# Kernel optimization log

Measured on AMD Instinct MI355X. Metric: run time of the kernel, lower is better.

Reference implementation:

```python
import jax, jax.numpy as jnp
import numpy as np

B, P, ENC = 64, 196, 512
E, H, A, V, L = 1024, 1024, 512, 20000, 25


def setup_inputs() -> dict:
    key = jax.random.key(0)
    ks = jax.random.split(key, 20)
    s = 0.02
    return {
        "encoder_out": jax.random.normal(ks[0], (B, P, ENC), jnp.float32),
        "captions": jax.random.randint(ks[1], (B, L), 0, V),
        "lengths": L,
        # attention MLP
        "W_enc_att": jax.random.normal(ks[2], (ENC, A), jnp.float32) * s,
        "b_enc_att": jnp.zeros((A,), jnp.float32),
        "W_dec_att": jax.random.normal(ks[3], (H, A), jnp.float32) * s,
        "b_dec_att": jnp.zeros((A,), jnp.float32),
        "W_full_att": jax.random.normal(ks[4], (A, 1), jnp.float32) * s,
        "b_full_att": jnp.zeros((1,), jnp.float32),
        # embedding
        "emb_table": jax.random.normal(ks[5], (V, E), jnp.float32) * s,
        # LSTMCell: input = embedding + context -> (E+ENC, 4H)
        "W_ih": jax.random.normal(ks[6], (E + ENC, 4 * H), jnp.float32) * s,
        "b_ih": jnp.zeros((4 * H,), jnp.float32),
        "W_hh": jax.random.normal(ks[7], (H, 4 * H), jnp.float32) * s,
        "b_hh": jnp.zeros((4 * H,), jnp.float32),
        # init states
        "W_init_h": jax.random.normal(ks[8], (ENC, H), jnp.float32) * s,
        "b_init_h": jnp.zeros((H,), jnp.float32),
        "W_init_c": jax.random.normal(ks[9], (ENC, H), jnp.float32) * s,
        "b_init_c": jnp.zeros((H,), jnp.float32),
        # gate + output proj
        "W_fbeta": jax.random.normal(ks[10], (H, ENC), jnp.float32) * s,
        "b_fbeta": jnp.zeros((ENC,), jnp.float32),
        "W_fc": jax.random.normal(ks[11], (H, V), jnp.float32) * s,
        "b_fc": jnp.zeros((V,), jnp.float32),
    }


def _decode(encoder_out, W_enc_att, b_enc_att, W_dec_att, b_dec_att,
            W_full_att, b_full_att, emb_table, W_ih, b_ih, W_hh, b_hh,
            W_init_h, b_init_h, W_init_c, b_init_c, W_fbeta, b_fbeta,
            W_fc, b_fc, captions, T):
    # precompute encoder-side attention projection (constant across timesteps)
    att_enc = encoder_out @ W_enc_att + b_enc_att          # (B, P, A)
    mean_feat = encoder_out.mean(axis=1)                   # (B, ENC)
    h0 = mean_feat @ W_init_h + b_init_h
    c0 = mean_feat @ W_init_c + b_init_c
    embeddings = emb_table[captions[:, :T]]                # (B, T, E)
    xs = jnp.swapaxes(embeddings, 0, 1)                    # (T, B, E)

    def step(carry, emb_t):
        h, c = carry
        att_dec = h @ W_dec_att + b_dec_att                # (B, A)
        energy = (jax.nn.relu(att_enc + att_dec[:, None, :]) @ W_full_att
                  + b_full_att)[..., 0]                    # (B, P)
        alpha = jax.nn.softmax(energy, axis=1)
        context = jnp.einsum('bp,bpe->be', alpha, encoder_out)
        gate = jax.nn.sigmoid(h @ W_fbeta + b_fbeta)       # (B, ENC)
        x = jnp.concatenate([emb_t, gate * context], axis=1)
        gates = x @ W_ih + b_ih + h @ W_hh + b_hh          # (B, 4H)
        i, f, g, o = jnp.split(gates, 4, axis=1)           # torch order i,f,g,o
        c = jax.nn.sigmoid(f) * c + jax.nn.sigmoid(i) * jnp.tanh(g)
        h = jax.nn.sigmoid(o) * jnp.tanh(c)
        preds = h @ W_fc + b_fc                            # dropout = identity (eval)
        return (h, c), (preds, alpha)

    _, (preds, alphas) = jax.lax.scan(step, (h0, c0), xs)
    predictions = jnp.swapaxes(preds, 0, 1)                # (B, T, V)
    alphas = jnp.swapaxes(alphas, 0, 1)                    # (B, T, P)
    return predictions, alphas


def reference(encoder_out, captions, lengths, W_enc_att, b_enc_att, W_dec_att,
              b_dec_att, W_full_att, b_full_att, emb_table, W_ih, b_ih, W_hh,
              b_hh, W_init_h, b_init_h, W_init_c, b_init_c, W_fbeta, b_fbeta,
              W_fc, b_fc):
    T = int(lengths) - 1
    return _decode(encoder_out, W_enc_att, b_enc_att, W_dec_att, b_dec_att,
                   W_full_att, b_full_att, emb_table, W_ih, b_ih, W_hh, b_hh,
                   W_init_h, b_init_h, W_init_c, b_init_c, W_fbeta, b_fbeta,
                   W_fc, b_fc, captions, T)
```

## Files before the change

kernel.cpp:

```cpp
#include <hip/hip_runtime.h>
#include <hip/hip_bf16.h>

#define BB 64
#define PP 196
#define ENCD 512
#define ED 1024
#define HD 1024
#define AD 512
#define VD 20000
#define TT 24
#define VPAD 20096
#define HOFF 32768

typedef __attribute__((ext_vector_type(8))) short short8;
typedef __attribute__((ext_vector_type(4))) short short4v;
typedef __attribute__((ext_vector_type(4))) float f32x4;

__device__ __forceinline__ float sigf(float x) { return 1.f / (1.f + __expf(-x)); }

__device__ __forceinline__ unsigned short f2bf(float f) {
    unsigned u = __builtin_bit_cast(unsigned, f);
    u = (u + 0x7FFFu + ((u >> 16) & 1u)) >> 16;
    return (unsigned short)u;
}
__device__ __forceinline__ void split2(float v, unsigned short& h, unsigned short& l) {
    h = f2bf(v);
    float hf = __builtin_bit_cast(float, ((unsigned)h) << 16);
    l = f2bf(v - hf);
}

__global__ __launch_bounds__(256) void split_w_kernel(
    const float* __restrict__ W, unsigned short* __restrict__ oh,
    unsigned short* __restrict__ ol, int N , int Npad, int coff,
    int Nlaunch, int rowoff, int perm) {
    int n = blockIdx.x * 256 + threadIdx.x;
    if (n >= Nlaunch) return;
    int kc = blockIdx.y;
    int src = perm ? ((n & 3) * 1024 + (n >> 2)) : n;
    short8 vh, vl;
    #pragma unroll
    for (int j = 0; j < 8; ++j) {
        float v = (src < N) ? W[(size_t)(rowoff + kc * 8 + j) * N + src] : 0.f;
        unsigned short h, l; split2(v, h, l);
        vh[j] = (short)h; vl[j] = (short)l;
    }
    size_t o = ((size_t)kc * Npad + coff + n) * 8;
    *(short8*)(oh + o) = vh; *(short8*)(ol + o) = vl;
}

__global__ __launch_bounds__(256) void embed_f32_kernel(
    const int* __restrict__ captions, const float* __restrict__ table,
    float* __restrict__ emb_f) {
    int t = blockIdx.x, b = blockIdx.y;
    int tok = captions[b * 25 + t];
    const float4* src = (const float4*)(table + (size_t)tok * ED);
    float4* dst = (float4*)(emb_f + ((size_t)t * BB + b) * ED);
    dst[threadIdx.x] = src[threadIdx.x];
}

__global__ __launch_bounds__(256) void bias_perm_kernel(
    const float* __restrict__ b_ih, const float* __restrict__ b_hh,
    float* __restrict__ out) {
    int n = blockIdx.x * 256 + threadIdx.x;
    int src = (n & 3) * 1024 + (n >> 2);
    out[n] = b_ih[src] + b_hh[src];
}

__global__ __launch_bounds__(512) void mean_kernel(const float* __restrict__ enc,
                                                   float* __restrict__ mf) {
    int b = blockIdx.x; int e = threadIdx.x;
    const float* base = enc + (size_t)b * PP * ENCD + e;
    float s = 0.f;
    #pragma unroll 4
    for (int p = 0; p < PP; ++p) s += base[(size_t)p * ENCD];
    mf[b * ENCD + e] = s * (1.f / PP);
}

__global__ __launch_bounds__(256) void init_hc_kernel(
    const float* __restrict__ mf,
    const float* __restrict__ Wh, const float* __restrict__ bh,
    const float* __restrict__ Wc, const float* __restrict__ bc,
    unsigned short* __restrict__ hc_h, unsigned short* __restrict__ hc_l,
    float* __restrict__ c0) {
    int b = blockIdx.x;
    int isC = blockIdx.y;
    const float* W    = isC ? Wc : Wh;
    const float* bias = isC ? bc : bh;
    __shared__ float smf[ENCD];
    for (int i = threadIdx.x; i < ENCD; i += 256) smf[i] = mf[b * ENCD + i];
    __syncthreads();
    #pragma unroll
    for (int jj = 0; jj < 4; ++jj) {
        int j = threadIdx.x + jj * 256;
        float acc = bias[j];
        for (int k = 0; k < ENCD; ++k) acc += smf[k] * W[(size_t)k * HD + j];
        if (isC) c0[b * HD + j] = acc;
        else {
            unsigned short h, l; split2(acc, h, l);
            size_t o = ((size_t)(j >> 3) * 64 + b) * 8 + (j & 7);
            hc_h[o] = h; hc_l[o] = l;
        }
    }
}

__global__ __launch_bounds__(256) void mfma_gemm_bigf(
    const float* __restrict__ Ap,
    const unsigned short* __restrict__ Bh, const unsigned short* __restrict__ Bl,
    const float* __restrict__ bias, float* __restrict__ C,
    int N, int Npad, int K, int Mtiles, int Ntiles, int inner_m) {
    __shared__ __align__(16) short lds[32768];
    short* Ahs = lds;
    short* Als = lds + 8192;
    short* Bhs = lds + 16384;
    short* Bls = lds + 24576;
    int tid = threadIdx.x, lane = tid & 63, w = tid >> 6;
    int nwg = Mtiles * Ntiles;
    int orig = blockIdx.x;
    int q = nwg >> 3, r = nwg & 7;
    int xcd = orig & 7;
    int basew = (xcd < r) ? xcd * (q + 1) : r * (q + 1) + (xcd - r) * q;
    int wg = basew + (orig >> 3);
    int mt, nt;
    if (inner_m) { mt = wg % Mtiles; nt = wg / Mtiles; }
    else         { nt = wg % Ntiles; mt = wg / Ntiles; }
    int m0 = mt * 128, n0 = nt * 128;
    int wr = w >> 1, wc = w & 1;
    f32x4 acc[4][4];
    #pragma unroll
    for (int i = 0; i < 4; ++i)
        #pragma unroll
        for (int j = 0; j < 4; ++j) acc[i][j] = (f32x4){0.f, 0.f, 0.f, 0.f};
    int nsteps = K >> 6;
    float4 va[8];
    short8 rb[2][4];
    auto load_step = [&](int s) {
        int k0 = s * 64, kc0 = s * 8;
        #pragma unroll
        for (int it = 0; it < 8; ++it) {
            int idx = it * 256 + tid; int m = idx >> 4, k4 = idx & 15;
            va[it] = *(const float4*)(Ap + (size_t)(m0 + m) * K + k0 + k4 * 4);
        }
        #pragma unroll
        for (int it = 0; it < 4; ++it) {
            int g = w * 4 + it; int kcl = g >> 1; int rb0 = (g & 1) * 64;
            size_t gb = ((size_t)(kc0 + kcl) * Npad + n0 + rb0 + lane) * 8;
            rb[0][it] = *(const short8*)(Bh + gb);
            rb[1][it] = *(const short8*)(Bl + gb);
        }
    };
    load_step(0);
    for (int s = 0; s < nsteps; ++s) {
        __syncthreads();
        #pragma unroll
        for (int it = 0; it < 8; ++it) {
            int idx = it * 256 + tid; int m = idx >> 4, k4 = idx & 15;
            int kc = k4 >> 1, jh = (k4 & 1) * 4;
            float vv[4] = {va[it].x, va[it].y, va[it].z, va[it].w};
            short4v hv, lv;
            #pragma unroll
            for (int qq = 0; qq < 4; ++qq) {
                unsigned short h, l; split2(vv[qq], h, l);
                hv[qq] = (short)h; lv[qq] = (short)l;
            }
            int o = kc * 1024 + ((m ^ kc) << 3) + jh;
            *(short4v*)(Ahs + o) = hv;
            *(short4v*)(Als + o) = lv;
        }
        #pragma unroll
        for (int it = 0; it < 4; ++it) {
            int g = w * 4 + it; int kcl = g >> 1; int rb0 = (g & 1) * 64;
            int o = (kcl * 128 + rb0 + lane) * 8;
            *(short8*)(Bhs + o) = rb[0][it];
            *(short8*)(Bls + o) = rb[1][it];
        }
        __syncthreads();
        if (s + 1 < nsteps) load_step(s + 1);
        #pragma unroll
        for (int ks = 0; ks < 2; ++ks) {
            int kq = ks * 4 + (lane >> 4);
            short8 afh[4], afl[4], bfh[4], bfl[4];
            #pragma unroll
            for (int mi = 0; mi < 4; ++mi) {
                int row = wr * 64 + mi * 16 + (lane & 15);
                int o = kq * 1024 + ((row ^ kq) << 3);
                afh[mi] = *(const short8*)(Ahs + o);
                afl[mi] = *(const short8*)(Als + o);
            }
            #pragma unroll
            for (int ni = 0; ni < 4; ++ni) {
                int o = (kq * 128 + wc * 64 + ni * 16 + (lane & 15)) * 8;
                bfh[ni] = *(const short8*)(Bhs + o);
                bfl[ni] = *(const short8*)(Bls + o);
            }
            #pragma unroll
            for (int mi = 0; mi < 4; ++mi)
                #pragma unroll
                for (int ni = 0; ni < 4; ++ni) {
                    acc[mi][ni] = __builtin_amdgcn_mfma_f32_16x16x32_bf16(afh[mi], bfh[ni], acc[mi][ni], 0, 0, 0);
                    acc[mi][ni] = __builtin_amdgcn_mfma_f32_16x16x32_bf16(afh[mi], bfl[ni], acc[mi][ni], 0, 0, 0);
                    acc[mi][ni] = __builtin_amdgcn_mfma_f32_16x16x32_bf16(afl[mi], bfh[ni], acc[mi][ni], 0, 0, 0);
                }
        }
    }
    #pragma unroll
    for (int mi = 0; mi < 4; ++mi) {
        int rrow = m0 + wr * 64 + mi * 16 + ((lane >> 4) << 2);
        #pragma unroll
        for (int ni = 0; ni < 4; ++ni) {
            int c = n0 + wc * 64 + ni * 16 + (lane & 15);
            if (c < N) {
                float bv = bias ? bias[c] : 0.f;
                #pragma unroll
                for (int qq = 0; qq < 4; ++qq)
                    C[(size_t)(rrow + qq) * N + c] = acc[mi][ni][qq] + bv;
            }
        }
    }
}

__global__ __launch_bounds__(256) void hgemm_direct(
    const unsigned short* __restrict__ Ah, const unsigned short* __restrict__ Al,
    const unsigned short* __restrict__ Bh, const unsigned short* __restrict__ Bl,
    float* __restrict__ out ) {
    int tid = threadIdx.x, lane = tid & 63, w = tid >> 6;
    int n0 = blockIdx.x * 128 + w * 32;
    int kc0 = blockIdx.y * 16;
    out += (size_t)blockIdx.y * 64 * 5120;
    f32x4 acc[4][2];
    #pragma unroll
    for (int i = 0; i < 4; ++i)
        #pragma unroll
        for (int j = 0; j < 2; ++j) acc[i][j] = (f32x4){0.f, 0.f, 0.f, 0.f};
    #pragma unroll
    for (int s = 0; s < 4; ++s) {
        int kc = kc0 + s * 4 + (lane >> 4);
        short8 afh[4], afl[4], bfh[2], bfl[2];
        #pragma unroll
        for (int mi = 0; mi < 4; ++mi) {
            size_t o = ((size_t)kc * 64 + mi * 16 + (lane & 15)) * 8;
            afh[mi] = *(const short8*)(Ah + o);
            afl[mi] = *(const short8*)(Al + o);
        }
        #pragma unroll
        for (int ni = 0; ni < 2; ++ni) {
            size_t o = ((size_t)kc * 5120 + n0 + ni * 16 + (lane & 15)) * 8;
            bfh[ni] = *(const short8*)(Bh + o);
            bfl[ni] = *(const short8*)(Bl + o);
        }
        #pragma unroll
        for (int mi = 0; mi < 4; ++mi)
            #pragma unroll
            for (int ni = 0; ni < 2; ++ni) {
                acc[mi][ni] = __builtin_amdgcn_mfma_f32_16x16x32_bf16(afh[mi], bfh[ni], acc[mi][ni], 0, 0, 0);
                acc[mi][ni] = __builtin_amdgcn_mfma_f32_16x16x32_bf16(afh[mi], bfl[ni], acc[mi][ni], 0, 0, 0);
                acc[mi][ni] = __builtin_amdgcn_mfma_f32_16x16x32_bf16(afl[mi], bfh[ni], acc[mi][ni], 0, 0, 0);
            }
    }
    #pragma unroll
    for (int mi = 0; mi < 4; ++mi) {
        int rrow = mi * 16 + ((lane >> 4) << 2);
        #pragma unroll
        for (int ni = 0; ni < 2; ++ni) {
            int c = n0 + ni * 16 + (lane & 15);
            #pragma unroll
            for (int qq = 0; qq < 4; ++qq)
                out[(size_t)(rrow + qq) * 5120 + c] = acc[mi][ni][qq];
        }
    }
}

__global__ __launch_bounds__(1024) void attn_ctx_kernel(
    const float* __restrict__ att_enc, const float* __restrict__ adg,
    const float* __restrict__ b_dec, const float* __restrict__ Wfull,
    const float* __restrict__ enc, const float* __restrict__ b_fbeta,
    float* __restrict__ alpha_out, unsigned short* __restrict__ x2h,
    unsigned short* __restrict__ x2l, int t) {
    int b = blockIdx.x; int tid = threadIdx.x;
    __shared__ float sdec[AD], sw[AD], sgate[AD], sal[256], sE[256], red[256];
    __shared__ float sctx[2][AD];
    if (tid < AD) {
        float s = b_dec[tid];
        #pragma unroll
        for (int ks = 0; ks < 8; ++ks) s += adg[((size_t)ks * BB + b) * 5120 + tid];
        sdec[tid] = s;
        sw[tid] = Wfull[tid];
    } else {
        int e = tid - AD;
        float s = b_fbeta[e];
        #pragma unroll
        for (int ks = 0; ks < 8; ++ks) s += adg[((size_t)ks * BB + b) * 5120 + 512 + e];
        sgate[e] = s;
    }
    __syncthreads();
    int w = tid >> 6, lane = tid & 63;
    float4 sd0 = *(const float4*)&sdec[lane * 8];
    float4 sd1 = *(const float4*)&sdec[lane * 8 + 4];
    float4 sw0 = *(const float4*)&sw[lane * 8];
    float4 sw1 = *(const float4*)&sw[lane * 8 + 4];
    for (int p = w; p < PP; p += 16) {
        const float* row = att_enc + ((size_t)b * PP + p) * AD + lane * 8;
        float4 v0 = *(const float4*)row;
        float4 v1 = *(const float4*)(row + 4);
        float part = fmaxf(v0.x + sd0.x, 0.f) * sw0.x + fmaxf(v0.y + sd0.y, 0.f) * sw0.y +
                     fmaxf(v0.z + sd0.z, 0.f) * sw0.z + fmaxf(v0.w + sd0.w, 0.f) * sw0.w +
                     fmaxf(v1.x + sd1.x, 0.f) * sw1.x + fmaxf(v1.y + sd1.y, 0.f) * sw1.y +
                     fmaxf(v1.z + sd1.z, 0.f) * sw1.z + fmaxf(v1.w + sd1.w, 0.f) * sw1.w;
        #pragma unroll
        for (int off = 32; off > 0; off >>= 1) part += __shfl_down(part, off, 64);
        if (lane == 0) sE[p] = part;
    }
    __syncthreads();
    float myE = (tid < PP) ? sE[tid] : -1e30f;
    if (tid < 256) red[tid] = myE;
    __syncthreads();
    for (int s = 128; s > 0; s >>= 1) {
        if (tid < s) red[tid] = fmaxf(red[tid], red[tid + s]);
        __syncthreads();
    }
    float mx = red[0];
    __syncthreads();
    float ex = (tid < PP) ? __expf(myE - mx) : 0.f;
    if (tid < 256) red[tid] = ex;
    __syncthreads();
    for (int s = 128; s > 0; s >>= 1) {
        if (tid < s) red[tid] += red[tid + s];
        __syncthreads();
    }
    if (tid < PP) {
        float al = ex * (1.f / red[0]);
        sal[tid] = al;
        alpha_out[((size_t)b * TT + t) * PP + tid] = al;
    }
    __syncthreads();
    int e = tid & 511, half = tid >> 9;
    const float* basep = enc + (size_t)b * PP * ENCD + e;
    float s2 = 0.f;
    #pragma unroll 2
    for (int p = half * 98; p < half * 98 + 98; ++p) s2 += sal[p] * basep[(size_t)p * ENCD];
    sctx[half][e] = s2;
    __syncthreads();
    if (tid < AD) {
        float ctx = sctx[0][tid] + sctx[1][tid];
        float gate = sigf(sgate[tid]);
        unsigned short h, l; split2(gate * ctx, h, l);
        size_t o = ((size_t)(tid >> 3) * 64 + b) * 8 + (tid & 7);
        x2h[o] = h; x2l[o] = l;
    }
}

__global__ __launch_bounds__(256) void gates_lstm2(
    const unsigned short* __restrict__ Ah, const unsigned short* __restrict__ Al,
    const unsigned short* __restrict__ Bh, const unsigned short* __restrict__ Bl,
    const float* __restrict__ pregates, const float* __restrict__ adg,
    float* __restrict__ c, unsigned short* __restrict__ ho_h,
    unsigned short* __restrict__ ho_l, float* __restrict__ h_all, int t) {
    __shared__ float gl[4][64][33];
    int tid = threadIdx.x, lane = tid & 63, w = tid >> 6;
    int n0 = blockIdx.x * 32;
    f32x4 acc[4][2];
    #pragma unroll
    for (int i = 0; i < 4; ++i)
        #pragma unroll
        for (int j = 0; j < 2; ++j) acc[i][j] = (f32x4){0.f, 0.f, 0.f, 0.f};
    #pragma unroll
    for (int s = 0; s < 4; ++s) {
        int kc = w * 16 + s * 4 + (lane >> 4);
        short8 afh[4], afl[4], bfh[2], bfl[2];
        #pragma unroll
        for (int mi = 0; mi < 4; ++mi) {
            size_t o = ((size_t)kc * 64 + mi * 16 + (lane & 15)) * 8;
            afh[mi] = *(const short8*)(Ah + o);
            afl[mi] = *(const short8*)(Al + o);
        }
        #pragma unroll
        for (int ni = 0; ni < 2; ++ni) {
            size_t o = ((size_t)kc * 4096 + n0 + ni * 16 + (lane & 15)) * 8;
            bfh[ni] = *(const short8*)(Bh + o);
            bfl[ni] = *(const short8*)(Bl + o);
        }
        #pragma unroll
        for (int mi = 0; mi < 4; ++mi)
            #pragma unroll
            for (int ni = 0; ni < 2; ++ni) {
                acc[mi][ni] = __builtin_amdgcn_mfma_f32_16x16x32_bf16(afh[mi], bfh[ni], acc[mi][ni], 0, 0, 0);
                acc[mi][ni] = __builtin_amdgcn_mfma_f32_16x16x32_bf16(afh[mi], bfl[ni], acc[mi][ni], 0, 0, 0);
                acc[mi][ni] = __builtin_amdgcn_mfma_f32_16x16x32_bf16(afl[mi], bfh[ni], acc[mi][ni], 0, 0, 0);
            }
    }
    #pragma unroll
    for (int mi = 0; mi < 4; ++mi) {
        int rrow = mi * 16 + ((lane >> 4) << 2);
        #pragma unroll
        for (int ni = 0; ni < 2; ++ni) {
            int cl = ni * 16 + (lane & 15);
            #pragma unroll
            for (int qq = 0; qq < 4; ++qq)
                gl[w][rrow + qq][cl] = acc[mi][ni][qq];
        }
    }
    __syncthreads();
    #pragma unroll
    for (int i = 0; i < 2; ++i) {
        int idx = tid + i * 256;
        int b = idx >> 3, jl = idx & 7;
        float g4[4];
        #pragma unroll
        for (int qq = 0; qq < 4; ++qq)
            g4[qq] = gl[0][b][4 * jl + qq] + gl[1][b][4 * jl + qq] +
                     gl[2][b][4 * jl + qq] + gl[3][b][4 * jl + qq];
        {
            float4 pv = *(const float4*)&pregates[((size_t)(t * 64 + b)) * 4096 + n0 + 4 * jl];
            g4[0] += pv.x; g4[1] += pv.y; g4[2] += pv.z; g4[3] += pv.w;
        }
        #pragma unroll
        for (int ks = 0; ks < 8; ++ks) {
            float4 av = *(const float4*)&adg[((size_t)ks * BB + b) * 5120 + 1024 + n0 + 4 * jl];
            g4[0] += av.x; g4[1] += av.y; g4[2] += av.z; g4[3] += av.w;
        }
        int j = (n0 >> 2) + jl;
        float cn = sigf(g4[1]) * c[b * HD + j] + sigf(g4[0]) * tanhf(g4[2]);
        c[b * HD + j] = cn;
        float hn = sigf(g4[3]) * tanhf(cn);
        unsigned short h, l; split2(hn, h, l);
        size_t o1 = ((size_t)(j >> 3) * 64 + b) * 8 + (j & 7);
        ho_h[o1] = h; ho_l[o1] = l;
        h_all[((size_t)b * TT + t) * HD + j] = hn;
    }
}

extern "C" void kernel_launch(void* const* d_in, const int* in_sizes, int n_in,
                              void* d_out, int out_size, void* d_ws, size_t ws_size,
                              hipStream_t stream) {
    const float* enc      = (const float*)d_in[0];
    const int*   captions = (const int*)d_in[1];
    const float* W_enc    = (const float*)d_in[3];
    const float* b_enc    = (const float*)d_in[4];
    const float* W_dec    = (const float*)d_in[5];
    const float* b_dec    = (const float*)d_in[6];
    const float* W_full   = (const float*)d_in[7];
    const float* table    = (const float*)d_in[9];
    const float* W_ih     = (const float*)d_in[10];
    const float* b_ih     = (const float*)d_in[11];
    const float* W_hh     = (const float*)d_in[12];
    const float* b_hh     = (const float*)d_in[13];
    const float* W_init_h = (const float*)d_in[14];
    const float* b_init_h = (const float*)d_in[15];
    const float* W_init_c = (const float*)d_in[16];
    const float* b_init_c = (const float*)d_in[17];
    const float* W_fbeta  = (const float*)d_in[18];
    const float* b_fbeta  = (const float*)d_in[19];
    const float* W_fc     = (const float*)d_in[20];
    const float* b_fc     = (const float*)d_in[21];

    float* preds  = (float*)d_out;
    float* alphas = (float*)d_out + (size_t)BB * TT * VD;

    char* base = (char*)d_ws;
    size_t off = 0;
    auto take = [&](size_t b) { void* r = (void*)(base + off); off += (b + 255) & ~(size_t)255; return r; };
    float* att_enc = (float*)take((size_t)12544 * 512 * 4);
    unsigned short* wbig_h = (unsigned short*)take((size_t)128 * 5120 * 8 * 2);
    unsigned short* wbig_l = (unsigned short*)take((size_t)128 * 5120 * 8 * 2);
    unsigned short* wih1_h = (unsigned short*)take((size_t)128 * 4096 * 8 * 2);
    unsigned short* wih1_l = (unsigned short*)take((size_t)128 * 4096 * 8 * 2);
    unsigned short* wih2_h = (unsigned short*)take((size_t)64 * 4096 * 8 * 2);
    unsigned short* wih2_l = (unsigned short*)take((size_t)64 * 4096 * 8 * 2);
    unsigned short* wenc_h = (unsigned short*)take((size_t)64 * 512 * 8 * 2);
    unsigned short* wenc_l = (unsigned short*)take((size_t)64 * 512 * 8 * 2);
    float* pregates = (float*)take((size_t)TT * BB * 4096 * 4);
    float* adg      = (float*)take((size_t)8 * BB * 5120 * 4);
    float* emb_f    = adg;
    float* biasp    = (float*)take((size_t)4096 * 4);
    unsigned short* wfc_h = (unsigned short*)(base);
    unsigned short* wfc_l = (unsigned short*)(base + (size_t)128 * VPAD * 8 * 2);
    float* c_buf = (float*)take((size_t)BB * HD * 4);
    float* mf    = (float*)take((size_t)BB * ENCD * 4);
    unsigned short* axh_h[2], *axh_l[2];
    axh_h[0] = (unsigned short*)take((size_t)192 * 64 * 8 * 2);
    axh_l[0] = (unsigned short*)take((size_t)192 * 64 * 8 * 2);
    axh_h[1] = (unsigned short*)take((size_t)192 * 64 * 8 * 2);
    axh_l[1] = (unsigned short*)take((size_t)192 * 64 * 8 * 2);
    float* h_all = (float*)take((size_t)TT * BB * HD * 4);

    split_w_kernel<<<dim3(2, 64), 256, 0, stream>>>(W_enc, wenc_h, wenc_l, 512, 512, 0, 512, 0, 0);
    split_w_kernel<<<dim3(2, 128), 256, 0, stream>>>(W_dec, wbig_h, wbig_l, 512, 5120, 0, 512, 0, 0);
    split_w_kernel<<<dim3(2, 128), 256, 0, stream>>>(W_fbeta, wbig_h, wbig_l, 512, 5120, 512, 512, 0, 0);
    split_w_kernel<<<dim3(16, 128), 256, 0, stream>>>(W_hh, wbig_h, wbig_l, 4096, 5120, 1024, 4096, 0, 1);
    split_w_kernel<<<dim3(16, 128), 256, 0, stream>>>(W_ih, wih1_h, wih1_l, 4096, 4096, 0, 4096, 0, 1);
    split_w_kernel<<<dim3(16, 64), 256, 0, stream>>>(W_ih, wih2_h, wih2_l, 4096, 4096, 0, 4096, 1024, 1);
    bias_perm_kernel<<<16, 256, 0, stream>>>(b_ih, b_hh, biasp);
    embed_f32_kernel<<<dim3(TT, BB), 256, 0, stream>>>(captions, table, emb_f);
    mean_kernel<<<BB, 512, 0, stream>>>(enc, mf);
    init_hc_kernel<<<dim3(BB, 2), 256, 0, stream>>>(mf, W_init_h, b_init_h, W_init_c, b_init_c,
                                                    axh_h[0] + HOFF, axh_l[0] + HOFF, c_buf);
    mfma_gemm_bigf<<<392, 256, 0, stream>>>(enc, wenc_h, wenc_l, b_enc, att_enc,
                                            512, 512, 512, 98, 4, 0);
    mfma_gemm_bigf<<<384, 256, 0, stream>>>(emb_f, wih1_h, wih1_l, biasp, pregates,
                                            4096, 4096, 1024, 12, 32, 1);

    for (int t = 0; t < TT; ++t) {
        int par = t & 1;
        hgemm_direct<<<dim3(40, 8), 256, 0, stream>>>(
            axh_h[par] + HOFF, axh_l[par] + HOFF, wbig_h, wbig_l, adg);
        attn_ctx_kernel<<<BB, 1024, 0, stream>>>(att_enc, adg, b_dec, W_full, enc, b_fbeta,
                                                 alphas, axh_h[par], axh_l[par], t);
        gates_lstm2<<<128, 256, 0, stream>>>(
            axh_h[par], axh_l[par], wih2_h, wih2_l, pregates, adg, c_buf,
            axh_h[1 - par] + HOFF, axh_l[1 - par] + HOFF, h_all, t);
    }

    split_w_kernel<<<dim3(79, 128), 256, 0, stream>>>(W_fc, wfc_h, wfc_l, VD, VPAD, 0, VPAD, 0, 0);
    mfma_gemm_bigf<<<1884, 256, 0, stream>>>(h_all, wfc_h, wfc_l, b_fc, preds,
                                             VD, VPAD, 1024, 12, 157, 1);
}
```

Measured before the change: 1.532 ms.

## Fuse per-timestep decoder kernels into one persistent cooperative kernel with grid syncs

Replaces the 72 per-timestep launches (hgemm, attention/context, gates+LSTM) with a single cooperative persistent kernel of 128 blocks that runs all timesteps and separates the phases with grid.sync(). It aims to remove kernel launch overhead and inter-kernel gaps in the sequential recurrence. The attention phase is split across two blocks per batch row, with the energy vector passing through a new global buffer. In exchange it adds four grid-wide barriers per step and runs on only 128 blocks. If the cooperative launch fails, it falls back to the old per-step launches.

After: 3.083 ms. 101% more time.

```diff
diff --git a/kernel.cpp b/kernel.cpp
--- a/kernel.cpp
+++ b/kernel.cpp
@@ -1,5 +1,8 @@
 #include <hip/hip_runtime.h>
 #include <hip/hip_bf16.h>
+#include <hip/hip_cooperative_groups.h>
+
+namespace cg = cooperative_groups;
 
 #define BB 64
 #define PP 196
@@ -31,7 +34,7 @@
 
 __global__ __launch_bounds__(256) void split_w_kernel(
     const float* __restrict__ W, unsigned short* __restrict__ oh,
-    unsigned short* __restrict__ ol, int N , int Npad, int coff,
+    unsigned short* __restrict__ ol, int N, int Npad, int coff,
     int Nlaunch, int rowoff, int perm) {
     int n = blockIdx.x * 256 + threadIdx.x;
     if (n >= Nlaunch) return;
@@ -221,7 +224,7 @@
 __global__ __launch_bounds__(256) void hgemm_direct(
     const unsigned short* __restrict__ Ah, const unsigned short* __restrict__ Al,
     const unsigned short* __restrict__ Bh, const unsigned short* __restrict__ Bl,
-    float* __restrict__ out ) {
+    float* __restrict__ out) {
     int tid = threadIdx.x, lane = tid & 63, w = tid >> 6;
     int n0 = blockIdx.x * 128 + w * 32;
     int kc0 = blockIdx.y * 16;
@@ -425,6 +428,234 @@
         size_t o1 = ((size_t)(j >> 3) * 64 + b) * 8 + (j & 7);
         ho_h[o1] = h; ho_l[o1] = l;
         h_all[((size_t)b * TT + t) * HD + j] = hn;
+    }
+}
+
+__global__ __launch_bounds__(512, 1) void step_kernel(
+    unsigned short* axh_h0, unsigned short* axh_l0,
+    unsigned short* axh_h1, unsigned short* axh_l1,
+    const unsigned short* __restrict__ wbig_h, const unsigned short* __restrict__ wbig_l,
+    const unsigned short* __restrict__ wih2_h, const unsigned short* __restrict__ wih2_l,
+    const float* __restrict__ att_enc, const float* __restrict__ enc,
+    const float* __restrict__ b_dec, const float* __restrict__ Wfull,
+    const float* __restrict__ b_fbeta, const float* __restrict__ pregates,
+    float* __restrict__ adg, float* __restrict__ eng,
+    float* __restrict__ c_buf, float* __restrict__ alphas,
+    float* __restrict__ h_all) {
+    cg::grid_group grid = cg::this_grid();
+    __shared__ __align__(16) float smem[8 * 64 * 33];
+    unsigned short* axh_h[2] = {axh_h0, axh_h1};
+    unsigned short* axh_l[2] = {axh_l0, axh_l1};
+    int bid = blockIdx.x, tid = threadIdx.x, lane = tid & 63, w = tid >> 6;
+
+    for (int t = 0; t < TT; ++t) {
+        int par = t & 1;
+        const unsigned short* hh = axh_h[par] + HOFF;
+        const unsigned short* hl = axh_l[par] + HOFF;
+        for (int u = 8 * bid + w; u < 1280; u += 1024) {
+            int ct = u % 160, ks = u / 160;
+            int n0 = ct * 32, kc0 = ks * 16;
+            f32x4 acc[4][2];
+            #pragma unroll
+            for (int i = 0; i < 4; ++i)
+                #pragma unroll
+                for (int j = 0; j < 2; ++j) acc[i][j] = (f32x4){0.f, 0.f, 0.f, 0.f};
+            #pragma unroll
+            for (int s = 0; s < 4; ++s) {
+                int kc = kc0 + s * 4 + (lane >> 4);
+                short8 afh[4], afl[4], bfh[2], bfl[2];
+                #pragma unroll
+                for (int mi = 0; mi < 4; ++mi) {
+                    size_t o = ((size_t)kc * 64 + mi * 16 + (lane & 15)) * 8;
+                    afh[mi] = *(const short8*)(hh + o);
+                    afl[mi] = *(const short8*)(hl + o);
+                }
+                #pragma unroll
+                for (int ni = 0; ni < 2; ++ni) {
+                    size_t o = ((size_t)kc * 5120 + n0 + ni * 16 + (lane & 15)) * 8;
+                    bfh[ni] = *(const short8*)(wbig_h + o);
+                    bfl[ni] = *(const short8*)(wbig_l + o);
+                }
+                #pragma unroll
+                for (int mi = 0; mi < 4; ++mi)
+                    #pragma unroll
+                    for (int ni = 0; ni < 2; ++ni) {
+                        acc[mi][ni] = __builtin_amdgcn_mfma_f32_16x16x32_bf16(afh[mi], bfh[ni], acc[mi][ni], 0, 0, 0);
+                        acc[mi][ni] = __builtin_amdgcn_mfma_f32_16x16x32_bf16(afh[mi], bfl[ni], acc[mi][ni], 0, 0, 0);
+                        acc[mi][ni] = __builtin_amdgcn_mfma_f32_16x16x32_bf16(afl[mi], bfh[ni], acc[mi][ni], 0, 0, 0);
+                    }
+            }
+            float* op = adg + (size_t)ks * 64 * 5120;
+            #pragma unroll
+            for (int mi = 0; mi < 4; ++mi) {
+                int rrow = mi * 16 + ((lane >> 4) << 2);
+                #pragma unroll
+                for (int ni = 0; ni < 2; ++ni) {
+                    int cc = n0 + ni * 16 + (lane & 15);
+                    #pragma unroll
+                    for (int qq = 0; qq < 4; ++qq)
+                        op[(size_t)(rrow + qq) * 5120 + cc] = acc[mi][ni][qq];
+                }
+            }
+        }
+        grid.sync();
+        {
+            int b = bid >> 1, half = bid & 1;
+            float* sdec = smem;
+            float* sw   = smem + 512;
+            if (tid < AD) {
+                float s = b_dec[tid];
+                #pragma unroll
+                for (int ks = 0; ks < 8; ++ks) s += adg[((size_t)ks * BB + b) * 5120 + tid];
+                sdec[tid] = s;
+                sw[tid] = Wfull[tid];
+            }
+            __syncthreads();
+            float4 sd0 = *(const float4*)&sdec[lane * 8];
+            float4 sd1 = *(const float4*)&sdec[lane * 8 + 4];
+            float4 sw0 = *(const float4*)&sw[lane * 8];
+            float4 sw1 = *(const float4*)&sw[lane * 8 + 4];
+            for (int p = half * 98 + w; p < half * 98 + 98; p += 8) {
+                const float* row = att_enc + ((size_t)b * PP + p) * AD + lane * 8;
+                float4 v0 = *(const float4*)row;
+                float4 v1 = *(const float4*)(row + 4);
+                float part = fmaxf(v0.x + sd0.x, 0.f) * sw0.x + fmaxf(v0.y + sd0.y, 0.f) * sw0.y +
+                             fmaxf(v0.z + sd0.z, 0.f) * sw0.z + fmaxf(v0.w + sd0.w, 0.f) * sw0.w +
+                             fmaxf(v1.x + sd1.x, 0.f) * sw1.x + fmaxf(v1.y + sd1.y, 0.f) * sw1.y +
+                             fmaxf(v1.z + sd1.z, 0.f) * sw1.z + fmaxf(v1.w + sd1.w, 0.f) * sw1.w;
+                #pragma unroll
+                for (int off = 32; off > 0; off >>= 1) part += __shfl_down(part, off, 64);
+                if (lane == 0) eng[b * PP + p] = part;
+            }
+        }
+        grid.sync();
+        {
+            int b = bid >> 1, half = bid & 1;
+            float* red  = smem + 1024;
+            float* sal  = smem + 1280;
+            float* sctx = smem + 1536;
+            float myE = (tid < PP) ? eng[b * PP + tid] : -1e30f;
+            if (tid < 256) red[tid] = myE;
+            __syncthreads();
+            for (int s = 128; s > 0; s >>= 1) {
+                if (tid < s) red[tid] = fmaxf(red[tid], red[tid + s]);
+                __syncthreads();
+            }
+            float mx = red[0];
+            __syncthreads();
+            float ex = (tid < PP) ? __expf(myE - mx) : 0.f;
+            if (tid < 256) red[tid] = ex;
+            __syncthreads();
+            for (int s = 128; s > 0; s >>= 1) {
+                if (tid < s) red[tid] += red[tid + s];
+                __syncthreads();
+            }
+            if (tid < PP) {
+                float al = ex * (1.f / red[0]);
+                sal[tid] = al;
+                if (half == 0) alphas[((size_t)b * TT + t) * PP + tid] = al;
+            }
+            __syncthreads();
+            int cl = tid & 255, pg = tid >> 8;
+            int e = half * 256 + cl;
+            const float* basep = enc + (size_t)b * PP * ENCD + e;
+            float s2 = 0.f;
+            #pragma unroll 2
+            for (int p = pg * 98; p < pg * 98 + 98; ++p) s2 += sal[p] * basep[(size_t)p * ENCD];
+            sctx[pg * 256 + cl] = s2;
+            __syncthreads();
+            if (tid < 256) {
+                int ee = half * 256 + tid;
+                float ctx = sctx[tid] + sctx[256 + tid];
+                float gpre = b_fbeta[ee];
+                #pragma unroll
+                for (int ks = 0; ks < 8; ++ks)
+                    gpre += adg[((size_t)ks * BB + b) * 5120 + 512 + ee];
+                float gate = sigf(gpre);
+                unsigned short h, l; split2(gate * ctx, h, l);
+                size_t o = ((size_t)(ee >> 3) * 64 + b) * 8 + (ee & 7);
+                axh_h[par][o] = h; axh_l[par][o] = l;
+            }
+            __syncthreads();
+        }
+        grid.sync();
+        {
+            float (*gl)[64][33] = (float(*)[64][33])smem;
+            const unsigned short* xh = axh_h[par];
+            const unsigned short* xl = axh_l[par];
+            int n0 = bid * 32;
+            f32x4 acc[4][2];
+            #pragma unroll
+            for (int i = 0; i < 4; ++i)
+                #pragma unroll
+                for (int j = 0; j < 2; ++j) acc[i][j] = (f32x4){0.f, 0.f, 0.f, 0.f};
+            #pragma unroll
+            for (int s = 0; s < 2; ++s) {
+                int kc = w * 8 + s * 4 + (lane >> 4);
+                short8 afh[4], afl[4], bfh[2], bfl[2];
+                #pragma unroll
+                for (int mi = 0; mi < 4; ++mi) {
+                    size_t o = ((size_t)kc * 64 + mi * 16 + (lane & 15)) * 8;
+                    afh[mi] = *(const short8*)(xh + o);
+                    afl[mi] = *(const short8*)(xl + o);
+                }
+                #pragma unroll
+                for (int ni = 0; ni < 2; ++ni) {
+                    size_t o = ((size_t)kc * 4096 + n0 + ni * 16 + (lane & 15)) * 8;
+                    bfh[ni] = *(const short8*)(wih2_h + o);
+                    bfl[ni] = *(const short8*)(wih2_l + o);
+                }
+                #pragma unroll
+                for (int mi = 0; mi < 4; ++mi)
+                    #pragma unroll
+                    for (int ni = 0; ni < 2; ++ni) {
+                        acc[mi][ni] = __builtin_amdgcn_mfma_f32_16x16x32_bf16(afh[mi], bfh[ni], acc[mi][ni], 0, 0, 0);
+                        acc[mi][ni] = __builtin_amdgcn_mfma_f32_16x16x32_bf16(afh[mi], bfl[ni], acc[mi][ni], 0, 0, 0);
+                        acc[mi][ni] = __builtin_amdgcn_mfma_f32_16x16x32_bf16(afl[mi], bfh[ni], acc[mi][ni], 0, 0, 0);
+                    }
+            }
+            #pragma unroll
+            for (int mi = 0; mi < 4; ++mi) {
+                int rrow = mi * 16 + ((lane >> 4) << 2);
+                #pragma unroll
+                for (int ni = 0; ni < 2; ++ni) {
+                    int cl = ni * 16 + (lane & 15);
+                    #pragma unroll
+                    for (int qq = 0; qq < 4; ++qq)
+                        gl[w][rrow + qq][cl] = acc[mi][ni][qq];
+                }
+            }
+            __syncthreads();
+            int b = tid >> 3, jl = tid & 7;
+            float g4[4];
+            #pragma unroll
+            for (int qq = 0; qq < 4; ++qq) {
+                float s = 0.f;
+                #pragma unroll
+                for (int p = 0; p < 8; ++p) s += gl[p][b][4 * jl + qq];
+                g4[qq] = s;
+            }
+            {
+                float4 pv = *(const float4*)&pregates[((size_t)(t * 64 + b)) * 4096 + n0 + 4 * jl];
+                g4[0] += pv.x; g4[1] += pv.y; g4[2] += pv.z; g4[3] += pv.w;
+            }
+            #pragma unroll
+            for (int ks = 0; ks < 8; ++ks) {
+                float4 av = *(const float4*)&adg[((size_t)ks * BB + b) * 5120 + 1024 + n0 + 4 * jl];
+                g4[0] += av.x; g4[1] += av.y; g4[2] += av.z; g4[3] += av.w;
+            }
+            int j = (n0 >> 2) + jl;
+            float cn = sigf(g4[1]) * c_buf[b * HD + j] + sigf(g4[0]) * tanhf(g4[2]);
+            c_buf[b * HD + j] = cn;
+            float hn = sigf(g4[3]) * tanhf(cn);
+            unsigned short h, l; split2(hn, h, l);
+            size_t o1 = ((size_t)(j >> 3) * 64 + b) * 8 + (j & 7);
+            unsigned short* oh = axh_h[1 - par] + HOFF;
+            unsigned short* ol = axh_l[1 - par] + HOFF;
+            oh[o1] = h; ol[o1] = l;
+            h_all[((size_t)b * TT + t) * HD + j] = hn;
+        }
+        grid.sync();
     }
 }
 
@@ -475,12 +706,12 @@
     unsigned short* wfc_l = (unsigned short*)(base + (size_t)128 * VPAD * 8 * 2);
     float* c_buf = (float*)take((size_t)BB * HD * 4);
     float* mf    = (float*)take((size_t)BB * ENCD * 4);
-    unsigned short* axh_h[2], *axh_l[2];
-    axh_h[0] = (unsigned short*)take((size_t)192 * 64 * 8 * 2);
-    axh_l[0] = (unsigned short*)take((size_t)192 * 64 * 8 * 2);
-    axh_h[1] = (unsigned short*)take((size_t)192 * 64 * 8 * 2);
-    axh_l[1] = (unsigned short*)take((size_t)192 * 64 * 8 * 2);
+    unsigned short* axh_h0 = (unsigned short*)take((size_t)192 * 64 * 8 * 2);
+    unsigned short* axh_l0 = (unsigned short*)take((size_t)192 * 64 * 8 * 2);
+    unsigned short* axh_h1 = (unsigned short*)take((size_t)192 * 64 * 8 * 2);
+    unsigned short* axh_l1 = (unsigned short*)take((size_t)192 * 64 * 8 * 2);
     float* h_all = (float*)take((size_t)TT * BB * HD * 4);
+    float* eng   = (float*)take((size_t)BB * PP * 4);
 
     split_w_kernel<<<dim3(2, 64), 256, 0, stream>>>(W_enc, wenc_h, wenc_l, 512, 512, 0, 512, 0, 0);
     split_w_kernel<<<dim3(2, 128), 256, 0, stream>>>(W_dec, wbig_h, wbig_l, 512, 5120, 0, 512, 0, 0);
@@ -492,21 +723,38 @@
     embed_f32_kernel<<<dim3(TT, BB), 256, 0, stream>>>(captions, table, emb_f);
     mean_kernel<<<BB, 512, 0, stream>>>(enc, mf);
     init_hc_kernel<<<dim3(BB, 2), 256, 0, stream>>>(mf, W_init_h, b_init_h, W_init_c, b_init_c,
-                                                    axh_h[0] + HOFF, axh_l[0] + HOFF, c_buf);
+                                                    axh_h0 + HOFF, axh_l0 + HOFF, c_buf);
     mfma_gemm_bigf<<<392, 256, 0, stream>>>(enc, wenc_h, wenc_l, b_enc, att_enc,
                                             512, 512, 512, 98, 4, 0);
     mfma_gemm_bigf<<<384, 256, 0, stream>>>(emb_f, wih1_h, wih1_l, biasp, pregates,
                                             4096, 4096, 1024, 12, 32, 1);
 
-    for (int t = 0; t < TT; ++t) {
-        int par = t & 1;
-        hgemm_direct<<<dim3(40, 8), 256, 0, stream>>>(
-            axh_h[par] + HOFF, axh_l[par] + HOFF, wbig_h, wbig_l, adg);
-        attn_ctx_kernel<<<BB, 1024, 0, stream>>>(att_enc, adg, b_dec, W_full, enc, b_fbeta,
-                                                 alphas, axh_h[par], axh_l[par], t);
-        gates_lstm2<<<128, 256, 0, stream>>>(
-            axh_h[par], axh_l[par], wih2_h, wih2_l, pregates, adg, c_buf,
-            axh_h[1 - par] + HOFF, axh_l[1 - par] + HOFF, h_all, t);
+    {
+        const float* enc_a = enc; const float* bdec_a = b_dec; const float* wfull_a = W_full;
+        const float* bfb_a = b_fbeta;
+        void* args[] = {
+            (void*)&axh_h0, (void*)&axh_l0, (void*)&axh_h1, (void*)&axh_l1,
+            (void*)&wbig_h, (void*)&wbig_l, (void*)&wih2_h, (void*)&wih2_l,
+            (void*)&att_enc, (void*)&enc_a, (void*)&bdec_a, (void*)&wfull_a,
+            (void*)&bfb_a, (void*)&pregates, (void*)&adg, (void*)&eng,
+            (void*)&c_buf, (void*)&alphas, (void*)&h_all
+        };
+        hipError_t cerr = hipLaunchCooperativeKernel((const void*)step_kernel,
+                                                     dim3(128), dim3(512), args, 0, stream);
+        if (cerr != hipSuccess) {
+            unsigned short* ah[2] = {axh_h0, axh_h1};
+            unsigned short* al[2] = {axh_l0, axh_l1};
+            for (int t = 0; t < TT; ++t) {
+                int par = t & 1;
+                hgemm_direct<<<dim3(40, 8), 256, 0, stream>>>(
+                    ah[par] + HOFF, al[par] + HOFF, wbig_h, wbig_l, adg);
+                attn_ctx_kernel<<<BB, 1024, 0, stream>>>(att_enc, adg, b_dec, W_full, enc,
+                                                         b_fbeta, alphas, ah[par], al[par], t);
+                gates_lstm2<<<128, 256, 0, stream>>>(
+                    ah[par], al[par], wih2_h, wih2_l, pregates, adg, c_buf,
+                    ah[1 - par] + HOFF, al[1 - par] + HOFF, h_all, t);
+            }
+        }
     }
 
     split_w_kernel<<<dim3(79, 128), 256, 0, stream>>>(W_fc, wfc_h, wfc_l, VD, VPAD, 0, VPAD, 0, 0);
```

## Merge setup kernels into one launch and read encoder features as bf16 in attention

Applied to the files above, without the earlier changes.

Folds the six weight-split launches plus the bias-permute and embedding-gather kernels into a single megasplit kernel that branches on block index, which cuts launch overhead. Adds a one-time conversion of encoder_out to bf16, stored in the wih1 buffer after that buffer has been consumed, so the per-step attention context reduction reads half the bytes. This drops precision in the context sum from fp32 to single bf16 values, where the rest of the code uses a hi/lo split.

New measurement: 1.525 ms. Within noise of the previous version (-0.5%).

```diff
diff --git a/kernel.cpp b/kernel.cpp
--- a/kernel.cpp
+++ b/kernel.cpp
@@ -28,14 +28,14 @@
     float hf = __builtin_bit_cast(float, ((unsigned)h) << 16);
     l = f2bf(v - hf);
 }
-
-__global__ __launch_bounds__(256) void split_w_kernel(
+__device__ __forceinline__ float bf2f(unsigned short u) {
+    return __builtin_bit_cast(float, ((unsigned)u) << 16);
+}
+
+__device__ __forceinline__ void split_store(
     const float* __restrict__ W, unsigned short* __restrict__ oh,
-    unsigned short* __restrict__ ol, int N , int Npad, int coff,
-    int Nlaunch, int rowoff, int perm) {
-    int n = blockIdx.x * 256 + threadIdx.x;
-    if (n >= Nlaunch) return;
-    int kc = blockIdx.y;
+    unsigned short* __restrict__ ol, int N, int Npad, int coff,
+    int rowoff, int perm, int kc, int n) {
     int src = perm ? ((n & 3) * 1024 + (n >> 2)) : n;
     short8 vh, vl;
     #pragma unroll
@@ -48,22 +48,68 @@
     *(short8*)(oh + o) = vh; *(short8*)(ol + o) = vl;
 }
 
-__global__ __launch_bounds__(256) void embed_f32_kernel(
-    const int* __restrict__ captions, const float* __restrict__ table,
-    float* __restrict__ emb_f) {
-    int t = blockIdx.x, b = blockIdx.y;
-    int tok = captions[b * 25 + t];
-    const float4* src = (const float4*)(table + (size_t)tok * ED);
-    float4* dst = (float4*)(emb_f + ((size_t)t * BB + b) * ED);
-    dst[threadIdx.x] = src[threadIdx.x];
-}
-
-__global__ __launch_bounds__(256) void bias_perm_kernel(
-    const float* __restrict__ b_ih, const float* __restrict__ b_hh,
-    float* __restrict__ out) {
+__global__ __launch_bounds__(256) void megasplit_kernel(
+    const float* __restrict__ W_enc, unsigned short* __restrict__ wenc_h, unsigned short* __restrict__ wenc_l,
+    const float* __restrict__ W_dec, const float* __restrict__ W_fbeta, const float* __restrict__ W_hh,
+    unsigned short* __restrict__ wbig_h, unsigned short* __restrict__ wbig_l,
+    const float* __restrict__ W_ih,
+    unsigned short* __restrict__ wih1_h, unsigned short* __restrict__ wih1_l,
+    unsigned short* __restrict__ wih2_h, unsigned short* __restrict__ wih2_l,
+    const float* __restrict__ b_ih, const float* __restrict__ b_hh, float* __restrict__ biasp,
+    const int* __restrict__ captions, const float* __restrict__ table, float* __restrict__ emb_f) {
+    int bid = blockIdx.x, tid = threadIdx.x;
+    if (bid < 128) {
+        int local = bid, xb = local & 1, kc = local >> 1;
+        split_store(W_enc, wenc_h, wenc_l, 512, 512, 0, 0, 0, kc, xb * 256 + tid);
+    } else if (bid < 384) {
+        int local = bid - 128, xb = local & 1, kc = local >> 1;
+        split_store(W_dec, wbig_h, wbig_l, 512, 5120, 0, 0, 0, kc, xb * 256 + tid);
+    } else if (bid < 640) {
+        int local = bid - 384, xb = local & 1, kc = local >> 1;
+        split_store(W_fbeta, wbig_h, wbig_l, 512, 5120, 512, 0, 0, kc, xb * 256 + tid);
+    } else if (bid < 2688) {
+        int local = bid - 640, xb = local & 15, kc = local >> 4;
+        split_store(W_hh, wbig_h, wbig_l, 4096, 5120, 1024, 0, 1, kc, xb * 256 + tid);
+    } else if (bid < 4736) {
+        int local = bid - 2688, xb = local & 15, kc = local >> 4;
+        split_store(W_ih, wih1_h, wih1_l, 4096, 4096, 0, 0, 1, kc, xb * 256 + tid);
+    } else if (bid < 5760) {
+        int local = bid - 4736, xb = local & 15, kc = local >> 4;
+        split_store(W_ih, wih2_h, wih2_l, 4096, 4096, 0, 1024, 1, kc, xb * 256 + tid);
+    } else if (bid < 5776) {
+        int n = (bid - 5760) * 256 + tid;
+        int src = (n & 3) * 1024 + (n >> 2);
+        biasp[n] = b_ih[src] + b_hh[src];
+    } else {
+        int local = bid - 5776;
+        int t = local >> 6, b = local & 63;
+        int tok = captions[b * 25 + t];
+        const float4* src = (const float4*)(table + (size_t)tok * ED);
+        float4* dst = (float4*)(emb_f + ((size_t)t * BB + b) * ED);
+        dst[tid] = src[tid];
+    }
+}
+
+__global__ __launch_bounds__(256) void enc2bf16_kernel(
+    const float* __restrict__ enc, unsigned short* __restrict__ encb) {
+    size_t idx = ((size_t)blockIdx.x * 256 + threadIdx.x) * 8;
+    float4 v0 = *(const float4*)(enc + idx);
+    float4 v1 = *(const float4*)(enc + idx + 4);
+    short8 o;
+    o[0] = (short)f2bf(v0.x); o[1] = (short)f2bf(v0.y);
+    o[2] = (short)f2bf(v0.z); o[3] = (short)f2bf(v0.w);
+    o[4] = (short)f2bf(v1.x); o[5] = (short)f2bf(v1.y);
+    o[6] = (short)f2bf(v1.z); o[7] = (short)f2bf(v1.w);
+    *(short8*)(encb + idx) = o;
+}
+
+__global__ __launch_bounds__(256) void split_w_kernel(
+    const float* __restrict__ W, unsigned short* __restrict__ oh,
+    unsigned short* __restrict__ ol, int N, int Npad, int coff,
+    int Nlaunch, int rowoff, int perm) {
     int n = blockIdx.x * 256 + threadIdx.x;
-    int src = (n & 3) * 1024 + (n >> 2);
-    out[n] = b_ih[src] + b_hh[src];
+    if (n >= Nlaunch) return;
+    split_store(W, oh, ol, N, Npad, coff, rowoff, perm, blockIdx.y, n);
 }
 
 __global__ __launch_bounds__(512) void mean_kernel(const float* __restrict__ enc,
@@ -221,7 +267,7 @@
 __global__ __launch_bounds__(256) void hgemm_direct(
     const unsigned short* __restrict__ Ah, const unsigned short* __restrict__ Al,
     const unsigned short* __restrict__ Bh, const unsigned short* __restrict__ Bl,
-    float* __restrict__ out ) {
+    float* __restrict__ out) {
     int tid = threadIdx.x, lane = tid & 63, w = tid >> 6;
     int n0 = blockIdx.x * 128 + w * 32;
     int kc0 = blockIdx.y * 16;
@@ -272,7 +318,7 @@
 __global__ __launch_bounds__(1024) void attn_ctx_kernel(
     const float* __restrict__ att_enc, const float* __restrict__ adg,
     const float* __restrict__ b_dec, const float* __restrict__ Wfull,
-    const float* __restrict__ enc, const float* __restrict__ b_fbeta,
+    const unsigned short* __restrict__ encb, const float* __restrict__ b_fbeta,
     float* __restrict__ alpha_out, unsigned short* __restrict__ x2h,
     unsigned short* __restrict__ x2l, int t) {
     int b = blockIdx.x; int tid = threadIdx.x;
@@ -333,10 +379,11 @@
     }
     __syncthreads();
     int e = tid & 511, half = tid >> 9;
-    const float* basep = enc + (size_t)b * PP * ENCD + e;
+    const unsigned short* basep = encb + (size_t)b * PP * ENCD + e;
     float s2 = 0.f;
     #pragma unroll 2
-    for (int p = half * 98; p < half * 98 + 98; ++p) s2 += sal[p] * basep[(size_t)p * ENCD];
+    for (int p = half * 98; p < half * 98 + 98; ++p)
+        s2 += sal[p] * bf2f(basep[(size_t)p * ENCD]);
     sctx[half][e] = s2;
     __syncthreads();
     if (tid < AD) {
@@ -463,6 +510,7 @@
     unsigned short* wbig_l = (unsigned short*)take((size_t)128 * 5120 * 8 * 2);
     unsigned short* wih1_h = (unsigned short*)take((size_t)128 * 4096 * 8 * 2);
     unsigned short* wih1_l = (unsigned short*)take((size_t)128 * 4096 * 8 * 2);
+    unsigned short* encb   = (unsigned short*)wih1_h;
     unsigned short* wih2_h = (unsigned short*)take((size_t)64 * 4096 * 8 * 2);
     unsigned short* wih2_l = (unsigned short*)take((size_t)64 * 4096 * 8 * 2);
     unsigned short* wenc_h = (unsigned short*)take((size_t)64 * 512 * 8 * 2);
@@ -475,38 +523,38 @@
     unsigned short* wfc_l = (unsigned short*)(base + (size_t)128 * VPAD * 8 * 2);
     float* c_buf = (float*)take((size_t)BB * HD * 4);
     float* mf    = (float*)take((size_t)BB * ENCD * 4);
-    unsigned short* axh_h[2], *axh_l[2];
-    axh_h[0] = (unsigned short*)take((size_t)192 * 64 * 8 * 2);
-    axh_l[0] = (unsigned short*)take((size_t)192 * 64 * 8 * 2);
-    axh_h[1] = (unsigned short*)take((size_t)192 * 64 * 8 * 2);
-    axh_l[1] = (unsigned short*)take((size_t)192 * 64 * 8 * 2);
+    unsigned short* axh_h0 = (unsigned short*)take((size_t)192 * 64 * 8 * 2);
+    unsigned short* axh_l0 = (unsigned short*)take((size_t)192 * 64 * 8 * 2);
+    unsigned short* axh_h1 = (unsigned short*)take((size_t)192 * 64 * 8 * 2);
+    unsigned short* axh_l1 = (unsigned short*)take((size_t)192 * 64 * 8 * 2);
     float* h_all = (float*)take((size_t)TT * BB * HD * 4);
 
-    split_w_kernel<<<dim3(2, 64), 256, 0, stream>>>(W_enc, wenc_h, wenc_l, 512, 512, 0, 512, 0, 0);
-    split_w_kernel<<<dim3(2, 128), 256, 0, stream>>>(W_dec, wbig_h, wbig_l, 512, 5120, 0, 512, 0, 0);
-    split_w_kernel<<<dim3(2, 128), 256, 0, stream>>>(W_fbeta, wbig_h, wbig_l, 512, 5120, 512, 512, 0, 0);
-    split_w_kernel<<<dim3(16, 128), 256, 0, stream>>>(W_hh, wbig_h, wbig_l, 4096, 5120, 1024, 4096, 0, 1);
-    split_w_kernel<<<dim3(16, 128), 256, 0, stream>>>(W_ih, wih1_h, wih1_l, 4096, 4096, 0, 4096, 0, 1);
-    split_w_kernel<<<dim3(16, 64), 256, 0, stream>>>(W_ih, wih2_h, wih2_l, 4096, 4096, 0, 4096, 1024, 1);
-    bias_perm_kernel<<<16, 256, 0, stream>>>(b_ih, b_hh, biasp);
-    embed_f32_kernel<<<dim3(TT, BB), 256, 0, stream>>>(captions, table, emb_f);
+    megasplit_kernel<<<7312, 256, 0, stream>>>(
+        W_enc, wenc_h, wenc_l, W_dec, W_fbeta, W_hh, wbig_h, wbig_l,
+        W_ih, wih1_h, wih1_l, wih2_h, wih2_l,
+        b_ih, b_hh, biasp, captions, table, emb_f);
     mean_kernel<<<BB, 512, 0, stream>>>(enc, mf);
     init_hc_kernel<<<dim3(BB, 2), 256, 0, stream>>>(mf, W_init_h, b_init_h, W_init_c, b_init_c,
-                                                    axh_h[0] + HOFF, axh_l[0] + HOFF, c_buf);
+                                                    axh_h0 + HOFF, axh_l0 + HOFF, c_buf);
     mfma_gemm_bigf<<<392, 256, 0, stream>>>(enc, wenc_h, wenc_l, b_enc, att_enc,
                                             512, 512, 512, 98, 4, 0);
     mfma_gemm_bigf<<<384, 256, 0, stream>>>(emb_f, wih1_h, wih1_l, biasp, pregates,
                                             4096, 4096, 1024, 12, 32, 1);
-
-    for (int t = 0; t < TT; ++t) {
-        int par = t & 1;
-        hgemm_direct<<<dim3(40, 8), 256, 0, stream>>>(
-            axh_h[par] + HOFF, axh_l[par] + HOFF, wbig_h, wbig_l, adg);
-        attn_ctx_kernel<<<BB, 1024, 0, stream>>>(att_enc, adg, b_dec, W_full, enc, b_fbeta,
-                                                 alphas, axh_h[par], axh_l[par], t);
-        gates_lstm2<<<128, 256, 0, stream>>>(
-            axh_h[par], axh_l[par], wih2_h, wih2_l, pregates, adg, c_buf,
-            axh_h[1 - par] + HOFF, axh_l[1 - par] + HOFF, h_all, t);
+    enc2bf16_kernel<<<3136, 256, 0, stream>>>(enc, encb);
+
+    {
+        unsigned short* ah[2] = {axh_h0, axh_h1};
+        unsigned short* al[2] = {axh_l0, axh_l1};
+        for (int t = 0; t < TT; ++t) {
+            int par = t & 1;
+            hgemm_direct<<<dim3(40, 8), 256, 0, stream>>>(
+                ah[par] + HOFF, al[par] + HOFF, wbig_h, wbig_l, adg);
+            attn_ctx_kernel<<<BB, 1024, 0, stream>>>(att_enc, adg, b_dec, W_full, encb,
+                                                     b_fbeta, alphas, ah[par], al[par], t);
+            gates_lstm2<<<128, 256, 0, stream>>>(
+                ah[par], al[par], wih2_h, wih2_l, pregates, adg, c_buf,
+                ah[1 - par] + HOFF, al[1 - par] + HOFF, h_all, t);
+        }
     }
 
     split_w_kernel<<<dim3(79, 128), 256, 0, stream>>>(W_fc, wfc_h, wfc_l, VD, VPAD, 0, VPAD, 0, 0);
```
